# Kernel optimization log

Hardware: AMD Instinct MI355X
Metric: run time of the kernel (lower is better)

Reference implementation:

```python
import jax, jax.numpy as jnp
import numpy as np
import math

# Module constants (from __init__ defaults / chosen init_kwargs)
B = 4            # hand_batch_size
C = 8            # num_cameras
BC = B * C       # camera batch
R = 256          # resolution
NB = 64          # num_bins
BIN = 0.0136     # bin_size
FOV = 33.0       # degrees
DCS = 0.001      # camera_sensor_distance
SIGMA_BIN = 3.0  # self.sigma for soft binning


def _masks():
    fov_rad = FOV * math.pi / 180.0
    scale = math.tan(fov_rad / 2.0)
    center_scale = scale * (1.0 - 1.0 / R)
    lin = jnp.linspace(-center_scale, center_scale, R, dtype=jnp.float32)
    xg, yg = jnp.meshgrid(lin, lin, indexing='xy')
    fm = jnp.stack([xg, -yg, -jnp.ones((R, R), jnp.float32)], axis=2)
    film_mask = -fm / jnp.linalg.norm(fm, axis=2, keepdims=True)  # [R,R,3]
    cos_mask = 1.0 / jnp.sqrt(xg * xg + yg * yg + 1.0)            # [R,R]
    return film_mask, cos_mask


def setup_inputs() -> dict:
    key = jax.random.key(0)
    k1, k2 = jax.random.split(key)
    film_mask, cos_mask = _masks()
    # per-pixel interpolated vertex normals (pre-normalization, as dr.interpolate output)
    normals = jax.random.normal(k1, (BC, R, R, 3), dtype=jnp.float32)
    # per-pixel camera-space intersection points; z ~ 0.5 m so depths fall mid-histogram
    intersections = jax.random.normal(k2, (BC, R, R, 3), dtype=jnp.float32) * 0.1 \
        + jnp.array([0.0, 0.0, 0.5], dtype=jnp.float32)
    return {"normals": normals, "intersections": intersections,
            "film_mask": film_mask, "cos_mask": cos_mask}


def reference(normals, intersections, film_mask, cos_mask):
    width = 2.0 * math.tan(FOV * math.pi / 360.0)
    # cosine foreshortening w.r.t. film ray directions
    dots = jnp.clip(jnp.einsum('ijk,bijk->bij', film_mask, normals), 0.0, 1.0)
    # laser origin offset by 2 * camera_sensor_distance along +x
    laser_points = intersections - jnp.array([2.0 * DCS, 0.0, 0.0], dtype=intersections.dtype)
    laser_distances = jnp.linalg.norm(laser_points, axis=3)  # [BC,R,R]
    laser_tan = jnp.sqrt(laser_points[..., 0] ** 2 + laser_points[..., 1] ** 2) / laser_points[..., 2]
    sig = math.tan(math.radians(21.5)) / 1.4
    laser_mask = jnp.exp(-laser_tan ** 2 / (2.0 * sig * sig))
    dots = dots * laser_mask
    radiance = dots / laser_distances / laser_distances / math.pi \
        * (width * width) * (cos_mask ** 3) / float(R * R)      # [BC,R,R]
    depths = (jnp.linalg.norm(intersections, axis=3) + laser_distances) / 2.0
    d_bin = depths / BIN                                         # [BC,R,R]
    b = jnp.arange(NB, dtype=jnp.float32)                        # [NB]
    # soft bin kernel: sigmoid(s*(d-b)) - sigmoid(s*(d-b-1)), [BC,R,R,NB]
    x = d_bin[..., None] - b
    kernels = jax.nn.sigmoid(SIGMA_BIN * x) - jax.nn.sigmoid(SIGMA_BIN * (x - 1.0))
    # histogram accumulation over all pixels -> per-camera transient [BC,NB]
    transients = jnp.einsum('bijk,bij->bk', kernels, radiance)
    return transients
```

## Files before the change

### kernel.cpp

```cpp
#include <hip/hip_runtime.h>
#include <math.h>

#define NPIX    65536
#define NBINS   64
#define NBATCH  32
#define SPLIT   32
#define BLOCKT  128
#define PXPT    4
#define ITERS   (NPIX / SPLIT / (BLOCKT * PXPT))
#define HSTRIDE 68
#define LDSN    (BLOCKT * HSTRIDE)
#define WIN     8

#define THREE_LOG2E 4.328085122666891f

__global__ __launch_bounds__(BLOCKT, 2) void spad_hist_kernel(
    const float* __restrict__ normals,
    const float* __restrict__ inters,
    const float* __restrict__ film,
    const float* __restrict__ cosm,
    float* __restrict__ ws,
    float kconst, float lmask_c, float half_inv_bin)
{
    __shared__ float hist[LDSN];
    const int tid = threadIdx.x;
    {
        float4* h4 = (float4*)&hist[tid * HSTRIDE];
        #pragma unroll
        for (int i = 0; i < HSTRIDE / 4; ++i) h4[i] = make_float4(0.f, 0.f, 0.f, 0.f);
    }
    __syncthreads();

    const int b = blockIdx.x & (NBATCH - 1);
    const int chunk = blockIdx.x / NBATCH;
    const int pix0 = chunk * (NPIX / SPLIT);
    const int base = tid * HSTRIDE;

    const float E3P[9] = {
        1.0f, 20.085536923187668f, 403.4287934927351f, 8103.083927575384f,
        162754.79141900392f, 3269017.372472111f, 65659969.13733051f,
        1318815734.4832146f, 26489122129.843472f };

    #pragma unroll
    for (int it = 0; it < ITERS; ++it) {
        const int pp = pix0 + (it * BLOCKT + tid) * PXPT;
        const float4* n4 = (const float4*)(normals + ((size_t)b * NPIX + pp) * 3);
        const float4* i4 = (const float4*)(inters  + ((size_t)b * NPIX + pp) * 3);
        const float4* f4 = (const float4*)(film + (size_t)pp * 3);
        const float4  c4 = *(const float4*)(cosm + pp);
        float4 n0 = n4[0], n1 = n4[1], n2 = n4[2];
        float4 i0 = i4[0], i1 = i4[1], i2 = i4[2];
        float4 f0 = f4[0], f1 = f4[1], f2 = f4[2];

        float NX[4] = {n0.x, n0.w, n1.z, n2.y}, NY[4] = {n0.y, n1.x, n1.w, n2.z},
              NZ[4] = {n0.z, n1.y, n2.x, n2.w};
        float IX[4] = {i0.x, i0.w, i1.z, i2.y}, IY[4] = {i0.y, i1.x, i1.w, i2.z},
              IZ[4] = {i0.z, i1.y, i2.x, i2.w};
        float FX[4] = {f0.x, f0.w, f1.z, f2.y}, FY[4] = {f0.y, f1.x, f1.w, f2.z},
              FZ[4] = {f0.z, f1.y, f2.x, f2.w};
        float CM[4] = {c4.x, c4.y, c4.z, c4.w};

        int   K0[4];
        float W[4][8];

        #pragma unroll
        for (int p = 0; p < 4; ++p) {
            float dt = FX[p] * NX[p] + FY[p] * NY[p] + FZ[p] * NZ[p];
            dt = fminf(fmaxf(dt, 0.0f), 1.0f);
            float lx = IX[p] - 0.002f;
            float lxy2 = lx * lx + IY[p] * IY[p];
            float l2 = lxy2 + IZ[p] * IZ[p];
            float ld = __builtin_amdgcn_sqrtf(l2);
            float lm = __builtin_amdgcn_exp2f(
                lmask_c * lxy2 * __builtin_amdgcn_rcpf(IZ[p] * IZ[p]));
            float cm3 = CM[p] * CM[p] * CM[p];
            float r = dt * lm * kconst * cm3 * __builtin_amdgcn_rcpf(l2);
            float di = __builtin_amdgcn_sqrtf(
                IX[p] * IX[p] + IY[p] * IY[p] + IZ[p] * IZ[p]);
            float d = (di + ld) * half_inv_bin;

            int j0 = (int)floorf(d);
            j0 = j0 < 3 ? 3 : (j0 > 59 ? 59 : j0);
            int k0 = (j0 - 3) & ~3;
            K0[p] = k0;
            float e0 = __builtin_amdgcn_exp2f(((float)k0 - d) * THREE_LOG2E);
            float S[9];
            #pragma unroll
            for (int m = 0; m < 9; ++m)
                S[m] = __builtin_amdgcn_rcpf(fmaf(e0, E3P[m], 1.0f));
            #pragma unroll
            for (int m = 0; m < 8; ++m)
                W[p][m] = r * (S[m] - S[m + 1]);
        }

        #pragma unroll
        for (int p = 0; p < 4; ++p) {
            float4* hp = (float4*)&hist[base + K0[p]];
            float4 a = hp[0], bb = hp[1];
            a.x  += W[p][0]; a.y  += W[p][1]; a.z  += W[p][2]; a.w  += W[p][3];
            bb.x += W[p][4]; bb.y += W[p][5]; bb.z += W[p][6]; bb.w += W[p][7];
            hp[0] = a; hp[1] = bb;
        }
    }
    __syncthreads();

    const int g = tid & 15;
    const int h = tid >> 4;
    float4 acc = make_float4(0.f, 0.f, 0.f, 0.f);
    #pragma unroll
    for (int j = 0; j < 16; ++j) {
        float4 v = *(const float4*)&hist[(h + 8 * j) * HSTRIDE + 4 * g];
        acc.x += v.x; acc.y += v.y; acc.z += v.z; acc.w += v.w;
    }
    __syncthreads();
    *(float4*)&hist[tid * 4] = acc;
    __syncthreads();
    if (tid < 16) {
        float4 s4 = make_float4(0.f, 0.f, 0.f, 0.f);
        #pragma unroll
        for (int hh = 0; hh < 8; ++hh) {
            float4 v = *(const float4*)&hist[hh * 64 + tid * 4];
            s4.x += v.x; s4.y += v.y; s4.z += v.z; s4.w += v.w;
        }
        *(float4*)&ws[(size_t)blockIdx.x * NBINS + tid * 4] = s4;
    }
}

__global__ __launch_bounds__(256) void spad_reduce_kernel(
    const float* __restrict__ ws, float* __restrict__ out)
{
    const int o = blockIdx.x * 256 + threadIdx.x;
    const int b = o >> 6;
    const int k = o & 63;
    float s = 0.0f;
    #pragma unroll
    for (int c = 0; c < SPLIT; ++c)
        s += ws[((size_t)(c * NBATCH + b)) * NBINS + k];
    out[o] = s;
}

extern "C" void kernel_launch(void* const* d_in, const int* in_sizes, int n_in,
                              void* d_out, int out_size, void* d_ws, size_t ws_size,
                              hipStream_t stream) {
    const float* normals = (const float*)d_in[0];
    const float* inters  = (const float*)d_in[1];
    const float* film    = (const float*)d_in[2];
    const float* cosm    = (const float*)d_in[3];
    float* out = (float*)d_out;
    float* ws  = (float*)d_ws;

    const double fov_rad = 33.0 * M_PI / 180.0;
    const double width = 2.0 * tan(fov_rad / 2.0);
    const double kconst_d = width * width / M_PI / 65536.0;
    const double sig = tan(21.5 * M_PI / 180.0) / 1.4;
    const double log2e = 1.4426950408889634;
    const double lmask_c_d = -log2e / (2.0 * sig * sig);
    const double half_inv_bin_d = 0.5 / 0.0136;

    spad_hist_kernel<<<NBATCH * SPLIT, BLOCKT, 0, stream>>>(
        normals, inters, film, cosm, ws,
        (float)kconst_d, (float)lmask_c_d, (float)half_inv_bin_d);

    spad_reduce_kernel<<<(NBATCH * NBINS) / 256, 256, 0, stream>>>(ws, out);
}
```

Baseline: 92.77 us.

## Prefetch next pixel batch into registers and widen soft-bin window to twelve

Adds register double-buffering: the next iteration's normals, intersections, film and cosine loads are issued before the current batch is computed, so global memory latency overlaps with the math. It also widens the per-pixel bin window from 8 to 12 bins, which means more sigmoid reciprocals and one more LDS read-modify-write per pixel. The window change improves accuracy coverage but adds ALU and LDS work. The prefetch raises register pressure, which could hurt occupancy at the 2-waves launch bound.

```diff
diff --git a/kernel.cpp b/kernel.cpp
--- a/kernel.cpp
+++ b/kernel.cpp
@@ -10,9 +10,11 @@
 #define ITERS   (NPIX / SPLIT / (BLOCKT * PXPT))
 #define HSTRIDE 68
 #define LDSN    (BLOCKT * HSTRIDE)
-#define WIN     8
+#define WIN     12
 
 #define THREE_LOG2E 4.328085122666891f
+
+struct Pix { float4 n0, n1, n2, i0, i1, i2, f0, f1, f2, c; };
 
 __global__ __launch_bounds__(BLOCKT, 2) void spad_hist_kernel(
     const float* __restrict__ normals,
@@ -36,32 +38,45 @@
     const int pix0 = chunk * (NPIX / SPLIT);
     const int base = tid * HSTRIDE;
 
-    const float E3P[9] = {
+    const float E3P[13] = {
         1.0f, 20.085536923187668f, 403.4287934927351f, 8103.083927575384f,
         162754.79141900392f, 3269017.372472111f, 65659969.13733051f,
-        1318815734.4832146f, 26489122129.843472f };
+        1318815734.4832146f, 26489122129.843472f, 532048240601.79865f,
+        10686474581524.462f, 214643579785916.06f, 4311231547115195.0f };
 
-    #pragma unroll
-    for (int it = 0; it < ITERS; ++it) {
+    auto loadPix = [&](int it) {
+        Pix P;
         const int pp = pix0 + (it * BLOCKT + tid) * PXPT;
         const float4* n4 = (const float4*)(normals + ((size_t)b * NPIX + pp) * 3);
         const float4* i4 = (const float4*)(inters  + ((size_t)b * NPIX + pp) * 3);
         const float4* f4 = (const float4*)(film + (size_t)pp * 3);
-        const float4  c4 = *(const float4*)(cosm + pp);
-        float4 n0 = n4[0], n1 = n4[1], n2 = n4[2];
-        float4 i0 = i4[0], i1 = i4[1], i2 = i4[2];
-        float4 f0 = f4[0], f1 = f4[1], f2 = f4[2];
+        P.n0 = n4[0]; P.n1 = n4[1]; P.n2 = n4[2];
+        P.i0 = i4[0]; P.i1 = i4[1]; P.i2 = i4[2];
+        P.f0 = f4[0]; P.f1 = f4[1]; P.f2 = f4[2];
+        P.c  = *(const float4*)(cosm + pp);
+        return P;
+    };
 
-        float NX[4] = {n0.x, n0.w, n1.z, n2.y}, NY[4] = {n0.y, n1.x, n1.w, n2.z},
-              NZ[4] = {n0.z, n1.y, n2.x, n2.w};
-        float IX[4] = {i0.x, i0.w, i1.z, i2.y}, IY[4] = {i0.y, i1.x, i1.w, i2.z},
-              IZ[4] = {i0.z, i1.y, i2.x, i2.w};
-        float FX[4] = {f0.x, f0.w, f1.z, f2.y}, FY[4] = {f0.y, f1.x, f1.w, f2.z},
-              FZ[4] = {f0.z, f1.y, f2.x, f2.w};
-        float CM[4] = {c4.x, c4.y, c4.z, c4.w};
+    Pix cur = loadPix(0);
+
+    #pragma unroll
+    for (int it = 0; it < ITERS; ++it) {
+        Pix nxt = cur;
+        if (it + 1 < ITERS) nxt = loadPix(it + 1);
+
+        float NX[4] = {cur.n0.x, cur.n0.w, cur.n1.z, cur.n2.y},
+              NY[4] = {cur.n0.y, cur.n1.x, cur.n1.w, cur.n2.z},
+              NZ[4] = {cur.n0.z, cur.n1.y, cur.n2.x, cur.n2.w};
+        float IX[4] = {cur.i0.x, cur.i0.w, cur.i1.z, cur.i2.y},
+              IY[4] = {cur.i0.y, cur.i1.x, cur.i1.w, cur.i2.z},
+              IZ[4] = {cur.i0.z, cur.i1.y, cur.i2.x, cur.i2.w};
+        float FX[4] = {cur.f0.x, cur.f0.w, cur.f1.z, cur.f2.y},
+              FY[4] = {cur.f0.y, cur.f1.x, cur.f1.w, cur.f2.z},
+              FZ[4] = {cur.f0.z, cur.f1.y, cur.f2.x, cur.f2.w};
+        float CM[4] = {cur.c.x, cur.c.y, cur.c.z, cur.c.w};
 
         int   K0[4];
-        float W[4][8];
+        float W[4][WIN];
 
         #pragma unroll
         for (int p = 0; p < 4; ++p) {
@@ -80,27 +95,30 @@
             float d = (di + ld) * half_inv_bin;
 
             int j0 = (int)floorf(d);
-            j0 = j0 < 3 ? 3 : (j0 > 59 ? 59 : j0);
-            int k0 = (j0 - 3) & ~3;
+            j0 = j0 < 4 ? 4 : (j0 > 56 ? 56 : j0);
+            int k0 = (j0 - 4) & ~3;
             K0[p] = k0;
             float e0 = __builtin_amdgcn_exp2f(((float)k0 - d) * THREE_LOG2E);
-            float S[9];
+            float S[WIN + 1];
             #pragma unroll
-            for (int m = 0; m < 9; ++m)
+            for (int m = 0; m < WIN + 1; ++m)
                 S[m] = __builtin_amdgcn_rcpf(fmaf(e0, E3P[m], 1.0f));
             #pragma unroll
-            for (int m = 0; m < 8; ++m)
+            for (int m = 0; m < WIN; ++m)
                 W[p][m] = r * (S[m] - S[m + 1]);
         }
 
         #pragma unroll
         for (int p = 0; p < 4; ++p) {
             float4* hp = (float4*)&hist[base + K0[p]];
-            float4 a = hp[0], bb = hp[1];
-            a.x  += W[p][0]; a.y  += W[p][1]; a.z  += W[p][2]; a.w  += W[p][3];
-            bb.x += W[p][4]; bb.y += W[p][5]; bb.z += W[p][6]; bb.w += W[p][7];
-            hp[0] = a; hp[1] = bb;
+            float4 a = hp[0], bb = hp[1], c = hp[2];
+            a.x  += W[p][0];  a.y  += W[p][1];  a.z  += W[p][2];  a.w  += W[p][3];
+            bb.x += W[p][4];  bb.y += W[p][5];  bb.z += W[p][6];  bb.w += W[p][7];
+            c.x  += W[p][8];  c.y  += W[p][9];  c.z  += W[p][10]; c.w  += W[p][11];
+            hp[0] = a; hp[1] = bb; hp[2] = c;
         }
+
+        cur = nxt;
     }
     __syncthreads();
 
```

New measurement: 95.11 us. 1.03x slower.
